# Kernel optimization log

Hardware: AMD Instinct MI355X
Metric: run time of the kernel (lower is better)

The kernel has to match this reference:

```python
import jax, jax.numpy as jnp
import numpy as np

THETA = 10000.0
EPS = 1e-6

def _rope_tables(n, d):
    # 2D image RoPE: square grid side x side, half of head-dim rotates with
    # row position, half with column position. rotate-half pairing (i, i+d/2).
    side = int(np.sqrt(n))
    dq = d // 4  # angle count per spatial axis
    inv_freq = 1.0 / (THETA ** (np.arange(dq, dtype=np.float32) / dq))
    ang = np.arange(side, dtype=np.float32)[:, None] * inv_freq[None, :]  # [side, dq]
    row = np.broadcast_to(ang[:, None, :], (side, side, dq)).reshape(n, dq)
    col = np.broadcast_to(ang[None, :, :], (side, side, dq)).reshape(n, dq)
    angles = np.concatenate([row, col], axis=-1)  # [n, d//2]
    return jnp.asarray(np.cos(angles)), jnp.asarray(np.sin(angles))

def _apply_rope(t, cos, sin):
    # t: [b, h, n, d]; cos/sin: [n, d//2]
    d2 = t.shape[-1] // 2
    t1, t2 = t[..., :d2], t[..., d2:]
    return jnp.concatenate([t1 * cos - t2 * sin, t1 * sin + t2 * cos], axis=-1)

def _rmsnorm(t, scale):
    var = jnp.mean(t * t, axis=-1, keepdims=True)
    return t * jax.lax.rsqrt(var + EPS) * scale

def setup_inputs() -> dict:
    key = jax.random.key(0)
    ks = jax.random.split(key, 3)
    B, N, D = 8, 1024, 1024
    x = jax.random.normal(ks[0], (B, N, D), dtype=jnp.float32)
    Wqkv = jax.random.normal(ks[1], (D, 3 * D), dtype=jnp.float32) * (D ** -0.5)
    bqkv = jnp.zeros((3 * D,), dtype=jnp.float32)
    Wout = jax.random.normal(ks[2], (D, D), dtype=jnp.float32) * (D ** -0.5)
    bout = jnp.zeros((D,), dtype=jnp.float32)
    hd = D // 16
    return {"x": x, "Wqkv": Wqkv, "bqkv": bqkv, "Wout": Wout, "bout": bout,
            "q_scale": jnp.ones((hd,), jnp.float32), "k_scale": jnp.ones((hd,), jnp.float32)}

def reference(x, Wqkv, bqkv, Wout, bout, q_scale, k_scale):
    B, N, D = x.shape
    H = 16
    hd = D // H
    qkv = x @ Wqkv + bqkv  # [B, N, 3D]
    qkv = qkv.reshape(B, N, 3, H, hd).transpose(2, 0, 3, 1, 4)  # [3, B, H, N, hd]
    q, k, v = qkv[0], qkv[1], qkv[2]
    q = _rmsnorm(q, q_scale)
    k = _rmsnorm(k, k_scale)
    cos, sin = _rope_tables(N, hd)
    q = _apply_rope(q, cos, sin)
    k = _apply_rope(k, cos, sin)
    scale = hd ** -0.5
    scores = jnp.einsum('bhqd,bhkd->bhqk', q, k) * scale
    attn = jax.nn.softmax(scores, axis=-1)
    o = jnp.einsum('bhqk,bhkd->bhqd', attn, v)  # [B, H, N, hd]
    o = o.transpose(0, 2, 1, 3).reshape(B, N, D)
    return o @ Wout + bout
```

## Files before the change

kernel.cpp:

```cpp
#include <hip/hip_runtime.h>
#include <hip/hip_bf16.h>
#include <hip/hip_fp16.h>
#include <math.h>

#define QSZ 8388608

typedef short bf16x8 __attribute__((ext_vector_type(8)));
typedef _Float16 f16x8 __attribute__((ext_vector_type(8)));
typedef _Float16 f16x4 __attribute__((ext_vector_type(4)));
typedef float f32x4 __attribute__((ext_vector_type(4)));

__device__ __forceinline__ unsigned short f2bf(float f) {
  __hip_bfloat16 h = __float2bfloat16(f);
  return *reinterpret_cast<unsigned short*>(&h);
}

__device__ __forceinline__ void gload16(const void* g, void* l) {
  __builtin_amdgcn_global_load_lds(
      (const __attribute__((address_space(1))) void*)g,
      (__attribute__((address_space(3))) void*)l, 16, 0, 0);
}

__global__ __launch_bounds__(256)
void cvt_all(const float* __restrict__ x, unsigned short* __restrict__ xb,
             const float* __restrict__ Wq, unsigned short* __restrict__ wqT,
             const float* __restrict__ Wo, unsigned short* __restrict__ woT) {
  __shared__ unsigned short tile[32][33];
  const int bid = blockIdx.x;
  const int t = threadIdx.x;
  if (bid < 4096) {
    const int i = (bid * 256 + t) * 8;
    const float4 a = *(const float4*)&x[i];
    const float4 b = *(const float4*)&x[i + 4];
    ushort4 lo, hi;
    lo.x = f2bf(a.x); lo.y = f2bf(a.y); lo.z = f2bf(a.z); lo.w = f2bf(a.w);
    hi.x = f2bf(b.x); hi.y = f2bf(b.y); hi.z = f2bf(b.z); hi.w = f2bf(b.w);
    *(ushort4*)&xb[i] = lo;
    *(ushort4*)&xb[i + 4] = hi;
    return;
  }
  const float* src;
  unsigned short* dst;
  int bx, by, N;
  if (bid < 7168) {
    src = Wq; dst = wqT; N = 3072;
    bx = (bid - 4096) % 96; by = (bid - 4096) / 96;
  } else {
    src = Wo; dst = woT; N = 1024;
    bx = (bid - 7168) % 32; by = (bid - 7168) / 32;
  }
  const int k0 = by * 32, n0 = bx * 32;
  const int r = t >> 3, c4 = (t & 7) * 4;
  const float4 v = *(const float4*)&src[(k0 + r) * N + n0 + c4];
  tile[r][c4 + 0] = f2bf(v.x);
  tile[r][c4 + 1] = f2bf(v.y);
  tile[r][c4 + 2] = f2bf(v.z);
  tile[r][c4 + 3] = f2bf(v.w);
  __syncthreads();
  ushort4 o;
  o.x = tile[c4 + 0][r];
  o.y = tile[c4 + 1][r];
  o.z = tile[c4 + 2][r];
  o.w = tile[c4 + 3][r];
  *(ushort4*)&dst[(long)(n0 + r) * 1024 + k0 + c4] = o;
}

template<int MODE>
__global__ __launch_bounds__(512, 2)
void gemm256(const unsigned short* __restrict__ A,
             const unsigned short* __restrict__ Bt,
             const float* __restrict__ bias,
             float* __restrict__ Cf,
             __half* __restrict__ Ch,
             const float* __restrict__ qsc,
             const float* __restrict__ ksc) {
  constexpr int BM  = (MODE == 0) ? 256 : 128;
  constexpr int AM  = (MODE == 0) ? 8 : 4;
  constexpr int LA  = BM / 64;
  constexpr int GXN = (MODE == 0) ? 12 : 4;
  constexpr int CPX = (MODE == 0) ? 48 : 32;

  __shared__ __align__(16) unsigned short As[2][BM * 64];
  __shared__ __align__(16) unsigned short Bs[2][16384];
  __shared__ float2 Tab[512];

  const int t = threadIdx.x;
  const int swz = (blockIdx.x & 7) * CPX + (blockIdx.x >> 3);
  const int bm = swz / GXN, bn = swz % GXN;
  const int w = t >> 6, lane = t & 63;
  const int M0 = (w >> 2) * (BM / 2), N0 = (w & 3) * 64;
  const int lm = lane & 15, q4 = lane >> 4;

  if (MODE == 0) {
    const int pos = t >> 4, idx = t & 15;
    const float invf = expf(-(float)idx * 0.57564627324851149f);
    const float ang = (float)pos * invf;
    Tab[t] = make_float2(cosf(ang), sinf(ang));
  }

  const int c8 = ((t & 7) ^ ((t >> 3) & 7)) << 3;
  const unsigned short* aSrc = A + (long)(bm * BM + (t >> 3)) * 1024 + c8;
  const unsigned short* bSrc = Bt + (long)(bn * 256 + (t >> 3)) * 1024 + c8;

  f32x4 acc[AM][4] = {};

  auto stage = [&](int buf, int kt) {
    const unsigned short* a = aSrc + kt * 64;
    const unsigned short* b = bSrc + kt * 64;
#pragma unroll
    for (int j = 0; j < LA; ++j)
      gload16(a + j * 65536, &As[buf][t * 8 + j * 4096]);
#pragma unroll
    for (int j = 0; j < 4; ++j)
      gload16(b + j * 65536, &Bs[buf][t * 8 + j * 4096]);
  };
  auto waitTile = [] {
    if constexpr (MODE == 0)
      asm volatile("s_waitcnt vmcnt(8)" ::: "memory");
    else
      asm volatile("s_waitcnt vmcnt(6)" ::: "memory");
  };

  auto compute = [&](const unsigned short* Ac, const unsigned short* Bc) {
#pragma unroll
    for (int kk = 0; kk < 2; ++kk) {
      bf16x8 af[AM], bg[4];
#pragma unroll
      for (int mi = 0; mi < AM; ++mi) {
        const int row = M0 + mi * 16 + lm;
        af[mi] = *(const bf16x8*)
            &Ac[row * 64 + ((((kk << 2) + q4) ^ (row & 7)) << 3)];
      }
#pragma unroll
      for (int ni = 0; ni < 4; ++ni) {
        const int row = N0 + ni * 16 + lm;
        bg[ni] = *(const bf16x8*)
            &Bc[row * 64 + ((((kk << 2) + q4) ^ (row & 7)) << 3)];
      }
#pragma unroll
      for (int mi = 0; mi < AM; ++mi)
#pragma unroll
        for (int ni = 0; ni < 4; ++ni)
          acc[mi][ni] = __builtin_amdgcn_mfma_f32_16x16x32_bf16(
              af[mi], bg[ni], acc[mi][ni], 0, 0, 0);
    }
  };

  stage(0, 0);
  stage(1, 1);
  waitTile();
  __builtin_amdgcn_s_barrier();

  for (int kt = 0; kt < 14; ++kt) {
    const int s = kt & 1;
    compute(s ? &As[1][0] : &As[0][0], s ? &Bs[1][0] : &Bs[0][0]);
    asm volatile("s_waitcnt lgkmcnt(0)" ::: "memory");
    __builtin_amdgcn_s_barrier();
    stage(s, kt + 2);
    waitTile();
    __builtin_amdgcn_s_barrier();
  }
  compute(&As[0][0], &Bs[0][0]);
  asm volatile("s_waitcnt lgkmcnt(0)" ::: "memory");
  __builtin_amdgcn_s_barrier();
  asm volatile("s_waitcnt vmcnt(0)" ::: "memory");
  __builtin_amdgcn_s_barrier();
  compute(&As[1][0], &Bs[1][0]);

  const int r0 = q4 << 2;
  const int nb = bn * 256 + N0;

  if (MODE == 1) {
#pragma unroll
    for (int mi = 0; mi < AM; ++mi)
#pragma unroll
      for (int ni = 0; ni < 4; ++ni) {
        const int n = nb + ni * 16 + lm;
        const float bvv = bias[n];
#pragma unroll
        for (int r = 0; r < 4; ++r)
          Cf[(long)(bm * BM + M0 + mi * 16 + r0 + r) * 1024 + n] =
              acc[mi][ni][r] + bvv;
      }
    return;
  }

  const int tq = nb >> 10, h = (nb >> 6) & 15;

  if (tq == 2) {
#pragma unroll
    for (int mi = 0; mi < AM; ++mi)
#pragma unroll
      for (int ni = 0; ni < 4; ++ni) {
        const int col = nb + ni * 16 + lm;
        const int dd = col & 63;
        const float bv = bias[col];
#pragma unroll
        for (int r = 0; r < 4; ++r) {
          const int m = bm * BM + M0 + mi * 16 + r0 + r;
          const int b = m >> 10, nn = m & 1023;
          Ch[2L * QSZ + ((long)((b * 16 + h) * 64 + dd)) * 1024 + nn] =
              __float2half(acc[mi][ni][r] + bv);
        }
      }
    return;
  }

  const float* scp = (tq == 0) ? qsc : ksc;
  const float qmul = (tq == 0) ? 0.18033688011112042f : 1.0f;
  float scv[4], bv[4];
#pragma unroll
  for (int ni = 0; ni < 4; ++ni) {
    scv[ni] = scp[ni * 16 + lm];
    bv[ni] = bias[nb + ni * 16 + lm];
  }
  __half* base = Ch + (long)tq * QSZ;
#pragma unroll
  for (int mi = 0; mi < AM; ++mi) {
#pragma unroll
    for (int r = 0; r < 4; ++r) {
      const float v0 = acc[mi][0][r] + bv[0];
      const float v1 = acc[mi][1][r] + bv[1];
      const float v2 = acc[mi][2][r] + bv[2];
      const float v3 = acc[mi][3][r] + bv[3];
      float ss = v0 * v0 + v1 * v1 + v2 * v2 + v3 * v3;
      ss += __shfl_xor(ss, 1, 64);
      ss += __shfl_xor(ss, 2, 64);
      ss += __shfl_xor(ss, 4, 64);
      ss += __shfl_xor(ss, 8, 64);
      const float inv = rsqrtf(ss * (1.0f / 64.0f) + 1e-6f) * qmul;
      const float a0 = v0 * inv * scv[0];
      const float a1 = v1 * inv * scv[1];
      const float a2 = v2 * inv * scv[2];
      const float a3 = v3 * inv * scv[3];
      const int m = bm * BM + M0 + mi * 16 + r0 + r;
      const int b = m >> 10, nn = m & 1023;
      const float2 tr = Tab[(nn >> 5) * 16 + lm];
      const float2 tc = Tab[(nn & 31) * 16 + lm];
      __half* row = base + ((long)((b * 16 + h) * 1024 + nn)) * 64 + lm;
      row[0]  = __float2half(a0 * tr.x - a2 * tr.y);
      row[16] = __float2half(a1 * tc.x - a3 * tc.y);
      row[32] = __float2half(a0 * tr.y + a2 * tr.x);
      row[48] = __float2half(a1 * tc.y + a3 * tc.x);
    }
  }
}

__global__ __launch_bounds__(256, 3)
void attn_mfma(const __half* __restrict__ qh, const __half* __restrict__ kh,
               const __half* __restrict__ vh, unsigned short* __restrict__ ob) {
  __shared__ __align__(16) __half Ks[2][4096];
  __shared__ __align__(16) __half Vs[2][4096];
  __shared__ __align__(16) __half Pl[8][1152];
  const int t = threadIdx.x;
  const int w = t >> 6, lane = t & 63;
  const int flat = blockIdx.x + blockIdx.y * 8;
  const int xcd = flat & 7, j = flat >> 3;
  const int bh = xcd * 16 + (j >> 3);
  const int qt = j & 7;
  const int lm = lane & 15, q4 = lane >> 4;

  f16x8 qf[2][2];
#pragma unroll
  for (int g = 0; g < 2; ++g) {
    const __half* qrow =
        qh + ((long)(bh * 1024 + qt * 128 + g * 64 + w * 16 + lm)) * 64 +
        q4 * 8;
    qf[g][0] = *(const f16x8*)qrow;
    qf[g][1] = *(const f16x8*)(qrow + 32);
  }

  f32x4 o[2][4] = {};
  float l_r[2] = {};

  const int prow = t >> 3, pc = t & 7;
  const int scz = pc ^ (prow & 7);
  const __half* ksrc0 = kh + (long)(bh * 1024 + prow) * 64 + scz * 8;
  const __half* vsrc0 = vh + (long)(bh * 64 + prow) * 1024 + scz * 8;

  gload16(ksrc0, &Ks[0][t * 8]);
  gload16(ksrc0 + 32 * 64, &Ks[0][2048 + t * 8]);
  gload16(vsrc0, &Vs[0][t * 8]);
  gload16(vsrc0 + 32 * 1024, &Vs[0][2048 + t * 8]);

  for (int kc = 0; kc < 16; ++kc) {
    const int cur = kc & 1;
    __syncthreads();

    if (kc < 15) {
      const int nx = cur ^ 1;
      const __half* ksrc = ksrc0 + (kc + 1) * 4096;
      const __half* vsrc = vsrc0 + (kc + 1) * 64;
      gload16(ksrc, &Ks[nx][t * 8]);
      gload16(ksrc + 32 * 64, &Ks[nx][2048 + t * 8]);
      gload16(vsrc, &Vs[nx][t * 8]);
      gload16(vsrc + 32 * 1024, &Vs[nx][2048 + t * 8]);
    }

    f16x8 kf[4][2];
#pragma unroll
    for (int nt = 0; nt < 4; ++nt) {
      const int kr = nt * 16 + lm;
#pragma unroll
      for (int ks = 0; ks < 2; ++ks)
        kf[nt][ks] = *(const f16x8*)&Ks[cur][kr * 64 +
                                      (((ks << 2) + q4) ^ (kr & 7)) * 8];
    }

#pragma unroll
    for (int g = 0; g < 2; ++g) {
      f32x4 s[4];
      __builtin_amdgcn_s_setprio(1);
#pragma unroll
      for (int nt = 0; nt < 4; ++nt) {
        s[nt] = (f32x4){0.f, 0.f, 0.f, 0.f};
#pragma unroll
        for (int ks = 0; ks < 2; ++ks)
          s[nt] = __builtin_amdgcn_mfma_f32_16x16x32_f16(kf[nt][ks], qf[g][ks],
                                                         s[nt], 0, 0, 0);
      }
      __builtin_amdgcn_s_setprio(0);
      __half* Pw = &Pl[w * 2 + g][0];
      float lacc = 0.f;
#pragma unroll
      for (int nt = 0; nt < 4; ++nt) {
        const float p0 = exp2f(s[nt][0] - 12.98425536800067f);
        const float p1 = exp2f(s[nt][1] - 12.98425536800067f);
        const float p2 = exp2f(s[nt][2] - 12.98425536800067f);
        const float p3 = exp2f(s[nt][3] - 12.98425536800067f);
        lacc += (p0 + p1) + (p2 + p3);
        f16x4 pv;
        pv[0] = (_Float16)p0; pv[1] = (_Float16)p1;
        pv[2] = (_Float16)p2; pv[3] = (_Float16)p3;
        *(f16x4*)&Pw[lm * 72 + nt * 16 + q4 * 4] = pv;
      }
      l_r[g] += lacc;
    }

    __builtin_amdgcn_s_setprio(1);
#pragma unroll
    for (int ks2 = 0; ks2 < 2; ++ks2) {
      const f16x8 pf0 = *(const f16x8*)&Pl[w * 2 + 0][lm * 72 + ks2 * 32 +
                                                      q4 * 8];
      const f16x8 pf1 = *(const f16x8*)&Pl[w * 2 + 1][lm * 72 + ks2 * 32 +
                                                      q4 * 8];
#pragma unroll
      for (int nt = 0; nt < 4; ++nt) {
        const int dr = nt * 16 + lm;
        const f16x8 vf = *(const f16x8*)&Vs[cur][dr * 64 +
                                          (((ks2 << 2) + q4) ^ (dr & 7)) * 8];
        o[0][nt] = __builtin_amdgcn_mfma_f32_16x16x32_f16(pf0, vf, o[0][nt],
                                                          0, 0, 0);
        o[1][nt] = __builtin_amdgcn_mfma_f32_16x16x32_f16(pf1, vf, o[1][nt],
                                                          0, 0, 0);
      }
    }
    __builtin_amdgcn_s_setprio(0);
  }

  const int b = bh >> 4, h = bh & 15;
#pragma unroll
  for (int g = 0; g < 2; ++g) {
    float l = l_r[g];
    l += __shfl_xor(l, 16, 64);
    l += __shfl_xor(l, 32, 64);
    const float linv_row = 1.0f / l;
#pragma unroll
    for (int r = 0; r < 4; ++r) {
      const float linv = __shfl(linv_row, q4 * 4 + r, 64);
      const long rowg =
          (long)(b * 1024 + qt * 128 + g * 64 + w * 16 + q4 * 4 + r) * 1024 +
          h * 64;
#pragma unroll
      for (int nt = 0; nt < 4; ++nt)
        ob[rowg + nt * 16 + lm] = f2bf(o[g][nt][r] * linv);
    }
  }
}

extern "C" void kernel_launch(void* const* d_in, const int* in_sizes, int n_in,
                              void* d_out, int out_size, void* d_ws,
                              size_t ws_size, hipStream_t stream) {
  const float* x    = (const float*)d_in[0];
  const float* Wqkv = (const float*)d_in[1];
  const float* bqkv = (const float*)d_in[2];
  const float* Wout = (const float*)d_in[3];
  const float* bout = (const float*)d_in[4];
  const float* qs   = (const float*)d_in[5];
  const float* ks   = (const float*)d_in[6];
  float* out = (float*)d_out;
  float* W = (float*)d_ws;

  __half* qkvh = (__half*)W;
  __half* qpre = qkvh;
  __half* kpre = qkvh + QSZ;
  __half* vT   = qkvh + 2 * QSZ;
  unsigned short* xb  = (unsigned short*)(W + 12582912);
  unsigned short* ob  = xb;
  unsigned short* wqT = (unsigned short*)(W + 16777216);
  unsigned short* woT = wqT + 3 * 1024 * 1024;

  cvt_all<<<8192, 256, 0, stream>>>(x, xb, Wqkv, wqT, Wout, woT);
  gemm256<0><<<384, 512, 0, stream>>>(xb, wqT, bqkv, nullptr, qkvh, qs, ks);
  attn_mfma<<<dim3(8, 128), 256, 0, stream>>>(qpre, kpre, vT, ob);
  gemm256<1><<<256, 512, 0, stream>>>(ob, woT, bout, out, nullptr, nullptr,
                                      nullptr);
}
```

Baseline: 252.9 us.

## Switch GEMM to triple-buffered BK=32 pipeline with one barrier per k-step

The GEMM main loop moves from a double-buffered 64-wide K tile with two barriers per step to a triple-buffered 32-wide K tile. The next-next stage load is issued between the LDS fragment reads and the MFMAs, so each iteration needs only one barrier. Block-to-tile mapping is also changed to group M tiles per XCD for L2 reuse, and the LDS swizzle is adapted to the narrower rows. The aim is to overlap global loads with compute and cut synchronisation. In exchange there are twice as many k-iterations and shallower MFMA work between barriers.

After: 247.7 us. 1.02x faster.

```diff
diff --git a/kernel.cpp b/kernel.cpp
--- a/kernel.cpp
+++ b/kernel.cpp
@@ -76,17 +76,17 @@
              const float* __restrict__ ksc) {
   constexpr int BM  = (MODE == 0) ? 256 : 128;
   constexpr int AM  = (MODE == 0) ? 8 : 4;
-  constexpr int LA  = BM / 64;
-  constexpr int GXN = (MODE == 0) ? 12 : 4;
-  constexpr int CPX = (MODE == 0) ? 48 : 32;
-
-  __shared__ __align__(16) unsigned short As[2][BM * 64];
-  __shared__ __align__(16) unsigned short Bs[2][16384];
+  constexpr int NT  = 32;
+
+  __shared__ __align__(16) unsigned short As[3][BM * 32];
+  __shared__ __align__(16) unsigned short Bs[3][8192];
   __shared__ float2 Tab[512];
 
   const int t = threadIdx.x;
-  const int swz = (blockIdx.x & 7) * CPX + (blockIdx.x >> 3);
-  const int bm = swz / GXN, bn = swz % GXN;
+  const int xcd = blockIdx.x & 7, c = blockIdx.x >> 3;
+  int bm, bn;
+  if (MODE == 0) { bm = xcd * 4 + (c & 3); bn = c >> 2; }
+  else           { bm = xcd * 8 + (c & 7); bn = c >> 3; }
   const int w = t >> 6, lane = t & 63;
   const int M0 = (w >> 2) * (BM / 2), N0 = (w & 3) * 64;
   const int lm = lane & 15, q4 = lane >> 4;
@@ -98,52 +98,25 @@
     Tab[t] = make_float2(cosf(ang), sinf(ang));
   }
 
-  const int c8 = ((t & 7) ^ ((t >> 3) & 7)) << 3;
-  const unsigned short* aSrc = A + (long)(bm * BM + (t >> 3)) * 1024 + c8;
-  const unsigned short* bSrc = Bt + (long)(bn * 256 + (t >> 3)) * 1024 + c8;
+  const int c8 = (((t & 3) ^ ((t >> 3) & 3)) << 3);
+  const unsigned short* aSrc = A + (long)(bm * BM + (t >> 2)) * 1024 + c8;
+  const unsigned short* bSrc = Bt + (long)(bn * 256 + (t >> 2)) * 1024 + c8;
 
   f32x4 acc[AM][4] = {};
 
   auto stage = [&](int buf, int kt) {
-    const unsigned short* a = aSrc + kt * 64;
-    const unsigned short* b = bSrc + kt * 64;
-#pragma unroll
-    for (int j = 0; j < LA; ++j)
-      gload16(a + j * 65536, &As[buf][t * 8 + j * 4096]);
-#pragma unroll
-    for (int j = 0; j < 4; ++j)
-      gload16(b + j * 65536, &Bs[buf][t * 8 + j * 4096]);
+    const unsigned short* a = aSrc + kt * 32;
+    const unsigned short* b = bSrc + kt * 32;
+    gload16(a, &As[buf][t * 8]);
+    if (MODE == 0) gload16(a + 128 * 1024, &As[buf][4096 + t * 8]);
+    gload16(b, &Bs[buf][t * 8]);
+    gload16(b + 128 * 1024, &Bs[buf][4096 + t * 8]);
   };
   auto waitTile = [] {
     if constexpr (MODE == 0)
-      asm volatile("s_waitcnt vmcnt(8)" ::: "memory");
+      asm volatile("s_waitcnt vmcnt(4)" ::: "memory");
     else
-      asm volatile("s_waitcnt vmcnt(6)" ::: "memory");
-  };
-
-  auto compute = [&](const unsigned short* Ac, const unsigned short* Bc) {
-#pragma unroll
-    for (int kk = 0; kk < 2; ++kk) {
-      bf16x8 af[AM], bg[4];
-#pragma unroll
-      for (int mi = 0; mi < AM; ++mi) {
-        const int row = M0 + mi * 16 + lm;
-        af[mi] = *(const bf16x8*)
-            &Ac[row * 64 + ((((kk << 2) + q4) ^ (row & 7)) << 3)];
-      }
-#pragma unroll
-      for (int ni = 0; ni < 4; ++ni) {
-        const int row = N0 + ni * 16 + lm;
-        bg[ni] = *(const bf16x8*)
-            &Bc[row * 64 + ((((kk << 2) + q4) ^ (row & 7)) << 3)];
-      }
-#pragma unroll
-      for (int mi = 0; mi < AM; ++mi)
-#pragma unroll
-        for (int ni = 0; ni < 4; ++ni)
-          acc[mi][ni] = __builtin_amdgcn_mfma_f32_16x16x32_bf16(
-              af[mi], bg[ni], acc[mi][ni], 0, 0, 0);
-    }
+      asm volatile("s_waitcnt vmcnt(3)" ::: "memory");
   };
 
   stage(0, 0);
@@ -151,21 +124,37 @@
   waitTile();
   __builtin_amdgcn_s_barrier();
 
-  for (int kt = 0; kt < 14; ++kt) {
-    const int s = kt & 1;
-    compute(s ? &As[1][0] : &As[0][0], s ? &Bs[1][0] : &Bs[0][0]);
-    asm volatile("s_waitcnt lgkmcnt(0)" ::: "memory");
-    __builtin_amdgcn_s_barrier();
-    stage(s, kt + 2);
-    waitTile();
-    __builtin_amdgcn_s_barrier();
-  }
-  compute(&As[0][0], &Bs[0][0]);
-  asm volatile("s_waitcnt lgkmcnt(0)" ::: "memory");
-  __builtin_amdgcn_s_barrier();
-  asm volatile("s_waitcnt vmcnt(0)" ::: "memory");
-  __builtin_amdgcn_s_barrier();
-  compute(&As[1][0], &Bs[1][0]);
+  for (int kt = 0; kt < NT; ++kt) {
+    const unsigned short* Ac = &As[kt % 3][0];
+    const unsigned short* Bc = &Bs[kt % 3][0];
+    bf16x8 af[AM], bg[4];
+#pragma unroll
+    for (int mi = 0; mi < AM; ++mi) {
+      const int row = M0 + mi * 16 + lm;
+      af[mi] = *(const bf16x8*)
+          &Ac[row * 32 + ((q4 ^ ((row >> 1) & 3)) << 3)];
+    }
+#pragma unroll
+    for (int ni = 0; ni < 4; ++ni) {
+      const int row = N0 + ni * 16 + lm;
+      bg[ni] = *(const bf16x8*)
+          &Bc[row * 32 + ((q4 ^ ((row >> 1) & 3)) << 3)];
+    }
+    if (kt < NT - 2) stage((kt + 2) % 3, kt + 2);
+#pragma unroll
+    for (int mi = 0; mi < AM; ++mi)
+#pragma unroll
+      for (int ni = 0; ni < 4; ++ni)
+        acc[mi][ni] = __builtin_amdgcn_mfma_f32_16x16x32_bf16(
+            af[mi], bg[ni], acc[mi][ni], 0, 0, 0);
+    if (kt < NT - 2) {
+      waitTile();
+      __builtin_amdgcn_s_barrier();
+    } else if (kt == NT - 2) {
+      asm volatile("s_waitcnt vmcnt(0)" ::: "memory");
+      __builtin_amdgcn_s_barrier();
+    }
+  }
 
   const int r0 = q4 << 2;
   const int nb = bn * 256 + N0;
```
